# Optimization experiments

Hardware: AMD Instinct MI355X
Metric: run time of the kernel (lower is better)

The kernel has to match this reference:

```python
import jax, jax.numpy as jnp
import numpy as np

EPS = 1e-06
N_HEADS = 16


def setup_inputs() -> dict:
    key = jax.random.key(0)
    k1, k2, k3 = jax.random.split(key, 3)
    B, T, C = 2, 2048, 1024
    x = jax.random.normal(k1, (B, T, C), dtype=jnp.float32)
    Wqkv = jax.random.normal(k2, (C, 3 * C), dtype=jnp.float32) * (1.0 / np.sqrt(C))
    Wout = jax.random.normal(k3, (C, C), dtype=jnp.float32) * (1.0 / np.sqrt(C))
    return {"x": x, "Wqkv": Wqkv, "Wout": Wout}


def reference(x, Wqkv, Wout):
    B, T, C = x.shape
    H = N_HEADS
    D = C // H
    qkv = x @ Wqkv  # [B,T,3C]
    q, k, v = jnp.split(qkv, 3, axis=-1)
    # [B,H,T,D]
    q = q.reshape(B, T, H, D).transpose(0, 2, 1, 3)
    k = k.reshape(B, T, H, D).transpose(0, 2, 1, 3)
    v = v.reshape(B, T, H, D).transpose(0, 2, 1, 3)
    dot = jnp.einsum('bhqd,bhkd->bhqk', q, k)
    qn = jnp.sum(q * q, axis=-1)[..., :, None]  # [B,H,T,1]
    kn = jnp.sum(k * k, axis=-1)[..., None, :]  # [B,H,1,T]
    scores = (dot * dot) / (qn + kn - 2.0 * dot + EPS)  # score_scale == 1.0
    causal = jnp.tril(jnp.ones((T, T), dtype=bool))  # [T,T]
    scores = jnp.where(causal[None, None], scores, -jnp.inf)
    attn = jax.nn.softmax(scores, axis=-1)
    out = jnp.einsum('bhqk,bhkd->bhqd', attn, v)
    out = out.transpose(0, 2, 1, 3).reshape(B, T, C)
    return out @ Wout
```

## Files before the change

### kernel.cpp

```cpp
#include <hip/hip_runtime.h>

#define T_SEQ   2048
#define C_DIM   1024
#define B_BATCH 2
#define H_HEADS 16
#define D_HEAD  64
#define EPS_Y   1e-6f

typedef short bf16x8 __attribute__((ext_vector_type(8)));
typedef float f32x4  __attribute__((ext_vector_type(4)));

__device__ __forceinline__ void split_bf16(float f, unsigned short& h, unsigned short& l) {
  unsigned int u = __float_as_uint(f);
  unsigned int hb = (u + 0x7fffu + ((u >> 16) & 1u)) >> 16;
  h = (unsigned short)hb;
  float hf = __uint_as_float(hb << 16);
  float res = f - hf;
  unsigned int v = __float_as_uint(res);
  l = (unsigned short)((v + 0x7fffu + ((v >> 16) & 1u)) >> 16);
}
__device__ __forceinline__ float bf2f(unsigned short u) {
  return __uint_as_float((unsigned int)u << 16);
}

__global__ __launch_bounds__(256) void convert_split(
    const float* __restrict__ in, unsigned short* __restrict__ hi,
    unsigned short* __restrict__ lo, int n4) {
  int idx = blockIdx.x * 256 + threadIdx.x;
  int stride = gridDim.x * 256;
  for (int i = idx; i < n4; i += stride) {
    float4 v = ((const float4*)in)[i];
    ushort4 h, l;
    split_bf16(v.x, h.x, l.x);
    split_bf16(v.y, h.y, l.y);
    split_bf16(v.z, h.z, l.z);
    split_bf16(v.w, h.w, l.w);
    ((ushort4*)hi)[i] = h;
    ((ushort4*)lo)[i] = l;
  }
}

__global__ __launch_bounds__(256) void transpose_split(
    const float* __restrict__ W, unsigned short* __restrict__ th,
    unsigned short* __restrict__ tl, int K, int N) {
  __shared__ float tile[64][65];
  const int bk = blockIdx.y * 64;
  const int bn = blockIdx.x * 64;
  const int t  = threadIdx.x;
  const int r  = t >> 2;
  const int c0 = (t & 3) << 4;

#pragma unroll
  for (int c = 0; c < 16; c += 4) {
    float4 v = *(const float4*)(W + (size_t)(bk + r) * N + bn + c0 + c);
    tile[r][c0 + c + 0] = v.x; tile[r][c0 + c + 1] = v.y;
    tile[r][c0 + c + 2] = v.z; tile[r][c0 + c + 3] = v.w;
  }
  __syncthreads();

#pragma unroll
  for (int c = 0; c < 16; c += 4) {
    ushort4 h, l;
    split_bf16(tile[c0 + c + 0][r], h.x, l.x);
    split_bf16(tile[c0 + c + 1][r], h.y, l.y);
    split_bf16(tile[c0 + c + 2][r], h.z, l.z);
    split_bf16(tile[c0 + c + 3][r], h.w, l.w);
    size_t off = (size_t)(bn + r) * K + bk + c0 + c;
    *(ushort4*)(th + off) = h;
    *(ushort4*)(tl + off) = l;
  }
}

template <bool BF16OUT>
__global__ __launch_bounds__(256) void gemm_split(
    const unsigned short* __restrict__ Ah, const unsigned short* __restrict__ Al,
    const unsigned short* __restrict__ Bh, const unsigned short* __restrict__ Bl,
    float* __restrict__ C, unsigned short* __restrict__ Ch,
    unsigned short* __restrict__ Cl, int M, int N, int K) {
  __shared__ alignas(16) short sAh[128][32], sAl[128][32];
  __shared__ alignas(16) short sBh[128][32], sBl[128][32];
  const int t  = threadIdx.x;
  const int l  = t & 63;
  const int w  = t >> 6;
  const int bm = blockIdx.y * 128;
  const int bn = blockIdx.x * 128;
  const int wm = (w >> 1) * 64;
  const int wn = (w & 1) * 64;

  f32x4 acc[4][4] = {};

  for (int k0 = 0; k0 < K; k0 += 32) {
#pragma unroll
    for (int r = 0; r < 2; ++r) {
      const int i   = r * 256 + t;
      const int row = i >> 2;
      const int k8  = (i & 3) << 3;
      const size_t ga = (size_t)(bm + row) * K + k0 + k8;
      const size_t gb = (size_t)(bn + row) * K + k0 + k8;
      *(bf16x8*)(&sAh[row][k8]) = *(const bf16x8*)(Ah + ga);
      *(bf16x8*)(&sAl[row][k8]) = *(const bf16x8*)(Al + ga);
      *(bf16x8*)(&sBh[row][k8]) = *(const bf16x8*)(Bh + gb);
      *(bf16x8*)(&sBl[row][k8]) = *(const bf16x8*)(Bl + gb);
    }
    __syncthreads();

    bf16x8 ah[4], al4[4], bh[4], bl4[4];
    const int lr = l & 15;
    const int kk = (l >> 4) << 3;
#pragma unroll
    for (int mi = 0; mi < 4; ++mi) {
      const int row = wm + mi * 16 + lr;
      ah[mi]  = *(const bf16x8*)(&sAh[row][kk]);
      al4[mi] = *(const bf16x8*)(&sAl[row][kk]);
    }
#pragma unroll
    for (int ni = 0; ni < 4; ++ni) {
      const int row = wn + ni * 16 + lr;
      bh[ni]  = *(const bf16x8*)(&sBh[row][kk]);
      bl4[ni] = *(const bf16x8*)(&sBl[row][kk]);
    }

#pragma unroll
    for (int mi = 0; mi < 4; ++mi)
#pragma unroll
      for (int ni = 0; ni < 4; ++ni) {
        acc[mi][ni] = __builtin_amdgcn_mfma_f32_16x16x32_bf16(ah[mi],  bh[ni],  acc[mi][ni], 0, 0, 0);
        acc[mi][ni] = __builtin_amdgcn_mfma_f32_16x16x32_bf16(ah[mi],  bl4[ni], acc[mi][ni], 0, 0, 0);
        acc[mi][ni] = __builtin_amdgcn_mfma_f32_16x16x32_bf16(al4[mi], bh[ni],  acc[mi][ni], 0, 0, 0);
      }
    __syncthreads();
  }

  const int cr = (l >> 4) << 2;
  const int cc = l & 15;
#pragma unroll
  for (int mi = 0; mi < 4; ++mi)
#pragma unroll
    for (int ni = 0; ni < 4; ++ni) {
      const size_t base = (size_t)(bm + wm + mi * 16 + cr) * N + bn + wn + ni * 16 + cc;
#pragma unroll
      for (int r = 0; r < 4; ++r) {
        if constexpr (BF16OUT) {
          unsigned short hu, lu;
          split_bf16(acc[mi][ni][r], hu, lu);
          Ch[base + (size_t)r * N] = hu;
          Cl[base + (size_t)r * N] = lu;
        } else {
          C[base + (size_t)r * N] = acc[mi][ni][r];
        }
      }
    }
}

__global__ __launch_bounds__(256, 4) void yat_attn_mfma(
    const unsigned short* __restrict__ qh, const unsigned short* __restrict__ ql,
    unsigned short* __restrict__ oh, unsigned short* __restrict__ ol) {
  const int qb = blockIdx.x;
  const int bh = blockIdx.y;
  const int b  = bh >> 4;
  const int h  = bh & 15;
  const size_t rs3 = 3 * C_DIM;
  const unsigned short* baseh = qh + (size_t)b * T_SEQ * rs3;
  const unsigned short* basel = ql + (size_t)b * T_SEQ * rs3;
  const int qcol = h * D_HEAD;
  const int kcol = C_DIM + h * D_HEAD;
  const int vcol = 2 * C_DIM + h * D_HEAD;

  __shared__ alignas(16) unsigned short Kh[64][72], Kl[64][72];
  __shared__ alignas(16) unsigned short Vth[64][72], Vtl[64][72];
  __shared__ float qn_row[64], kn_row[64];

  const int t = threadIdx.x;
  const int l = t & 63;
  const int w = t >> 6;
  const int lr   = l & 15;
  const int kk0  = (l >> 4) << 3;
  const int rgrp = (l >> 4) << 2;

  {
    const int row = t >> 2;
    const int d0  = (t & 3) << 4;
    const size_t g = (size_t)(qb * 64 + row) * rs3 + qcol + d0;
    bf16x8 h0 = *(const bf16x8*)(baseh + g);
    bf16x8 h1 = *(const bf16x8*)(baseh + g + 8);
    bf16x8 l0 = *(const bf16x8*)(basel + g);
    bf16x8 l1 = *(const bf16x8*)(basel + g + 8);
    *(bf16x8*)(&Kh[row][d0])     = h0;
    *(bf16x8*)(&Kh[row][d0 + 8]) = h1;
    *(bf16x8*)(&Kl[row][d0])     = l0;
    *(bf16x8*)(&Kl[row][d0 + 8]) = l1;
    float s = 0.f;
#pragma unroll
    for (int i = 0; i < 8; ++i) {
      float f0 = bf2f((unsigned short)h0[i]) + bf2f((unsigned short)l0[i]);
      float f1 = bf2f((unsigned short)h1[i]) + bf2f((unsigned short)l1[i]);
      s = fmaf(f0, f0, s);
      s = fmaf(f1, f1, s);
    }
    s += __shfl_xor(s, 1);
    s += __shfl_xor(s, 2);
    if ((t & 3) == 0) qn_row[row] = s;
  }

  const int ar = w * 16 + lr;
  bf16x8 qa_h0 = *(const bf16x8*)(&Kh[ar][kk0]);
  bf16x8 qa_h1 = *(const bf16x8*)(&Kh[ar][32 + kk0]);
  bf16x8 qa_l0 = *(const bf16x8*)(&Kl[ar][kk0]);
  bf16x8 qa_l1 = *(const bf16x8*)(&Kl[ar][32 + kk0]);

  float m_r[4] = {-INFINITY, -INFINITY, -INFINITY, -INFINITY};
  float l_r[4] = {0.f, 0.f, 0.f, 0.f};
  f32x4 o_acc[4] = {};
  float qn4[4];
#pragma unroll
  for (int r = 0; r < 4; ++r) qn4[r] = 0.f;

  __syncthreads();
#pragma unroll
  for (int r = 0; r < 4; ++r) qn4[r] = qn_row[w * 16 + rgrp + r];

  for (int kb = 0; kb <= qb; ++kb) {
    {
      const int row = t >> 2;
      const int d0  = (t & 3) << 4;
      const size_t g = (size_t)(kb * 64 + row) * rs3 + kcol + d0;
      bf16x8 h0 = *(const bf16x8*)(baseh + g);
      bf16x8 h1 = *(const bf16x8*)(baseh + g + 8);
      bf16x8 l0 = *(const bf16x8*)(basel + g);
      bf16x8 l1 = *(const bf16x8*)(basel + g + 8);
      *(bf16x8*)(&Kh[row][d0])     = h0;
      *(bf16x8*)(&Kh[row][d0 + 8]) = h1;
      *(bf16x8*)(&Kl[row][d0])     = l0;
      *(bf16x8*)(&Kl[row][d0 + 8]) = l1;
      float s = 0.f;
#pragma unroll
      for (int i = 0; i < 8; ++i) {
        float f0 = bf2f((unsigned short)h0[i]) + bf2f((unsigned short)l0[i]);
        float f1 = bf2f((unsigned short)h1[i]) + bf2f((unsigned short)l1[i]);
        s = fmaf(f0, f0, s);
        s = fmaf(f1, f1, s);
      }
      s += __shfl_xor(s, 1);
      s += __shfl_xor(s, 2);
      if ((t & 3) == 0) kn_row[row] = s;
    }
    {
      const int vj = l;
      const int d0 = w * 16;
      const size_t g = (size_t)(kb * 64 + vj) * rs3 + vcol + d0;
      bf16x8 h0 = *(const bf16x8*)(baseh + g);
      bf16x8 h1 = *(const bf16x8*)(baseh + g + 8);
      bf16x8 l0 = *(const bf16x8*)(basel + g);
      bf16x8 l1 = *(const bf16x8*)(basel + g + 8);
#pragma unroll
      for (int i = 0; i < 8; ++i) {
        Vth[d0 + i][vj]     = (unsigned short)h0[i];
        Vth[d0 + 8 + i][vj] = (unsigned short)h1[i];
        Vtl[d0 + i][vj]     = (unsigned short)l0[i];
        Vtl[d0 + 8 + i][vj] = (unsigned short)l1[i];
      }
    }
    __syncthreads();

    f32x4 s_acc[4] = {};
#pragma unroll
    for (int jt = 0; jt < 4; ++jt) {
      const int br = jt * 16 + lr;
      bf16x8 b_h0 = *(const bf16x8*)(&Kh[br][kk0]);
      bf16x8 b_h1 = *(const bf16x8*)(&Kh[br][32 + kk0]);
      bf16x8 b_l0 = *(const bf16x8*)(&Kl[br][kk0]);
      bf16x8 b_l1 = *(const bf16x8*)(&Kl[br][32 + kk0]);
      s_acc[jt] = __builtin_amdgcn_mfma_f32_16x16x32_bf16(qa_h0, b_h0, s_acc[jt], 0, 0, 0);
      s_acc[jt] = __builtin_amdgcn_mfma_f32_16x16x32_bf16(qa_h0, b_l0, s_acc[jt], 0, 0, 0);
      s_acc[jt] = __builtin_amdgcn_mfma_f32_16x16x32_bf16(qa_l0, b_h0, s_acc[jt], 0, 0, 0);
      s_acc[jt] = __builtin_amdgcn_mfma_f32_16x16x32_bf16(qa_h1, b_h1, s_acc[jt], 0, 0, 0);
      s_acc[jt] = __builtin_amdgcn_mfma_f32_16x16x32_bf16(qa_h1, b_l1, s_acc[jt], 0, 0, 0);
      s_acc[jt] = __builtin_amdgcn_mfma_f32_16x16x32_bf16(qa_l1, b_h1, s_acc[jt], 0, 0, 0);
    }

    {
      const bool diag = (kb == qb);
      const int gq0 = qb * 64 + w * 16 + rgrp;
#pragma unroll
      for (int jt = 0; jt < 4; ++jt) {
        const float kn = kn_row[jt * 16 + lr];
        const int gk = kb * 64 + jt * 16 + lr;
#pragma unroll
        for (int r = 0; r < 4; ++r) {
          const float dot = s_acc[jt][r];
          float sc = (dot * dot) / (qn4[r] + kn - 2.f * dot + EPS_Y);
          if (diag && gk > gq0 + r) sc = -INFINITY;
          s_acc[jt][r] = sc;
        }
      }
    }

    float scale[4];
#pragma unroll
    for (int r = 0; r < 4; ++r) {
      float mm = fmaxf(fmaxf(s_acc[0][r], s_acc[1][r]),
                       fmaxf(s_acc[2][r], s_acc[3][r]));
      mm = fmaxf(mm, __shfl_xor(mm, 1));
      mm = fmaxf(mm, __shfl_xor(mm, 2));
      mm = fmaxf(mm, __shfl_xor(mm, 4));
      mm = fmaxf(mm, __shfl_xor(mm, 8));
      const float mnew = fmaxf(m_r[r], mm);
      scale[r] = __expf(m_r[r] - mnew);
      m_r[r] = mnew;
    }
#pragma unroll
    for (int r = 0; r < 4; ++r) {
      float lsum = 0.f;
#pragma unroll
      for (int jt = 0; jt < 4; ++jt) {
        float p = __expf(s_acc[jt][r] - m_r[r]);
        s_acc[jt][r] = p;
        lsum += p;
      }
      lsum += __shfl_xor(lsum, 1);
      lsum += __shfl_xor(lsum, 2);
      lsum += __shfl_xor(lsum, 4);
      lsum += __shfl_xor(lsum, 8);
      l_r[r] = l_r[r] * scale[r] + lsum;
    }
#pragma unroll
    for (int dt = 0; dt < 4; ++dt)
#pragma unroll
      for (int r = 0; r < 4; ++r) o_acc[dt][r] *= scale[r];

    __syncthreads();

#pragma unroll
    for (int jt = 0; jt < 4; ++jt)
#pragma unroll
      for (int r = 0; r < 4; ++r) {
        unsigned short hu, lu;
        split_bf16(s_acc[jt][r], hu, lu);
        const int prow = w * 16 + rgrp + r;
        Kh[prow][jt * 16 + lr] = hu;
        Kl[prow][jt * 16 + lr] = lu;
      }

    {
      bf16x8 pa_h0 = *(const bf16x8*)(&Kh[ar][kk0]);
      bf16x8 pa_h1 = *(const bf16x8*)(&Kh[ar][32 + kk0]);
      bf16x8 pa_l0 = *(const bf16x8*)(&Kl[ar][kk0]);
      bf16x8 pa_l1 = *(const bf16x8*)(&Kl[ar][32 + kk0]);
#pragma unroll
      for (int dt = 0; dt < 4; ++dt) {
        const int vr = dt * 16 + lr;
        bf16x8 v_h0 = *(const bf16x8*)(&Vth[vr][kk0]);
        bf16x8 v_h1 = *(const bf16x8*)(&Vth[vr][32 + kk0]);
        bf16x8 v_l0 = *(const bf16x8*)(&Vtl[vr][kk0]);
        bf16x8 v_l1 = *(const bf16x8*)(&Vtl[vr][32 + kk0]);
        o_acc[dt] = __builtin_amdgcn_mfma_f32_16x16x32_bf16(pa_h0, v_h0, o_acc[dt], 0, 0, 0);
        o_acc[dt] = __builtin_amdgcn_mfma_f32_16x16x32_bf16(pa_h0, v_l0, o_acc[dt], 0, 0, 0);
        o_acc[dt] = __builtin_amdgcn_mfma_f32_16x16x32_bf16(pa_l0, v_h0, o_acc[dt], 0, 0, 0);
        o_acc[dt] = __builtin_amdgcn_mfma_f32_16x16x32_bf16(pa_h1, v_h1, o_acc[dt], 0, 0, 0);
        o_acc[dt] = __builtin_amdgcn_mfma_f32_16x16x32_bf16(pa_h1, v_l1, o_acc[dt], 0, 0, 0);
        o_acc[dt] = __builtin_amdgcn_mfma_f32_16x16x32_bf16(pa_l1, v_h1, o_acc[dt], 0, 0, 0);
      }
    }
    __syncthreads();
  }

  float inv[4];
#pragma unroll
  for (int r = 0; r < 4; ++r) inv[r] = 1.f / l_r[r];
#pragma unroll
  for (int dt = 0; dt < 4; ++dt)
#pragma unroll
    for (int r = 0; r < 4; ++r) {
      float v = o_acc[dt][r] * inv[r];
      unsigned short hu, lu;
      split_bf16(v, hu, lu);
      const size_t off = ((size_t)b * T_SEQ + qb * 64 + w * 16 + rgrp + r) * C_DIM
                         + h * D_HEAD + dt * 16 + lr;
      oh[off] = hu;
      ol[off] = lu;
    }
}

extern "C" void kernel_launch(void* const* d_in, const int* in_sizes, int n_in,
                              void* d_out, int out_size, void* d_ws, size_t ws_size,
                              hipStream_t stream) {
  const float* x    = (const float*)d_in[0];
  const float* Wqkv = (const float*)d_in[1];
  const float* Wout = (const float*)d_in[2];
  float* outp = (float*)d_out;

  const int M  = B_BATCH * T_SEQ;
  const int C3 = 3 * C_DIM;

  unsigned short* xh   = (unsigned short*)d_ws;
  unsigned short* xl   = xh   + (size_t)M * C_DIM;
  unsigned short* wqh  = xl   + (size_t)M * C_DIM;
  unsigned short* wql  = wqh  + (size_t)C_DIM * C3;
  unsigned short* woh  = wql  + (size_t)C_DIM * C3;
  unsigned short* wol  = woh  + (size_t)C_DIM * C_DIM;
  unsigned short* qkvh = wol  + (size_t)C_DIM * C_DIM;
  unsigned short* qkvl = qkvh + (size_t)M * C3;
  unsigned short* ath  = qkvl + (size_t)M * C3;
  unsigned short* atl  = ath  + (size_t)M * C_DIM;

  convert_split<<<2048, 256, 0, stream>>>(x, xh, xl, M * C_DIM / 4);
  {
    dim3 g1(C3 / 64, C_DIM / 64);
    transpose_split<<<g1, 256, 0, stream>>>(Wqkv, wqh, wql, C_DIM, C3);
    dim3 g2(C_DIM / 64, C_DIM / 64);
    transpose_split<<<g2, 256, 0, stream>>>(Wout, woh, wol, C_DIM, C_DIM);
  }
  {
    dim3 grid(C3 / 128, M / 128);
    gemm_split<true><<<grid, 256, 0, stream>>>(xh, xl, wqh, wql,
                                               nullptr, qkvh, qkvl, M, C3, C_DIM);
  }
  {
    dim3 grid(T_SEQ / 64, B_BATCH * H_HEADS);
    yat_attn_mfma<<<grid, 256, 0, stream>>>(qkvh, qkvl, ath, atl);
  }
  {
    dim3 grid(C_DIM / 128, M / 128);
    gemm_split<false><<<grid, 256, 0, stream>>>(ath, atl, woh, wol,
                                                outp, nullptr, nullptr, M, C_DIM, C_DIM);
  }
  (void)in_sizes; (void)n_in; (void)out_size; (void)ws_size;
}
```

Measured before the change: 457.4 us.

## Pair causal query tiles per block and precompute row norms in separate kernel

Each attention block now processes two query tiles (qb and 31-qb) so the causal work per block is balanced, halving the grid. Query and key squared norms are computed once by a new row_norms kernel into workspace (reusing the x split buffer) instead of being recomputed per key tile in every block. Q fragments load directly from global into registers, and the score division uses a fast reciprocal. The trade-offs are fewer blocks (512) with longer serial loops, which can reduce occupancy and latency hiding, plus an extra kernel launch.

```diff
diff --git a/kernel.cpp b/kernel.cpp
--- a/kernel.cpp
+++ b/kernel.cpp
@@ -68,6 +68,39 @@
     size_t off = (size_t)(bn + r) * K + bk + c0 + c;
     *(ushort4*)(th + off) = h;
     *(ushort4*)(tl + off) = l;
+  }
+}
+
+__global__ __launch_bounds__(256) void row_norms(
+    const unsigned short* __restrict__ qkvh, const unsigned short* __restrict__ qkvl,
+    float* __restrict__ qnG, float* __restrict__ knG) {
+  const int t    = threadIdx.x;
+  const int g    = blockIdx.x * 16 + (t >> 4);
+  const int lane = t & 15;
+  const int h    = g & (H_HEADS - 1);
+  const int bt   = g >> 4;
+  const int b    = bt >> 11;
+  const int trow = bt & (T_SEQ - 1);
+  const size_t rowbase = (size_t)bt * (3 * C_DIM);
+  const size_t outi = ((size_t)(b * H_HEADS + h)) * T_SEQ + trow;
+
+#pragma unroll
+  for (int plane = 0; plane < 2; ++plane) {
+    const size_t off = rowbase + (plane ? C_DIM : 0) + h * D_HEAD + lane * 4;
+    ushort4 hh = *(const ushort4*)(qkvh + off);
+    ushort4 ll = *(const ushort4*)(qkvl + off);
+    float f0 = bf2f(hh.x) + bf2f(ll.x);
+    float f1 = bf2f(hh.y) + bf2f(ll.y);
+    float f2 = bf2f(hh.z) + bf2f(ll.z);
+    float f3 = bf2f(hh.w) + bf2f(ll.w);
+    float s = f0 * f0 + f1 * f1 + f2 * f2 + f3 * f3;
+    s += __shfl_xor(s, 1);
+    s += __shfl_xor(s, 2);
+    s += __shfl_xor(s, 4);
+    s += __shfl_xor(s, 8);
+    if (lane == 0) {
+      if (plane == 0) qnG[outi] = s; else knG[outi] = s;
+    }
   }
 }
 
@@ -154,21 +187,22 @@
 
 __global__ __launch_bounds__(256, 4) void yat_attn_mfma(
     const unsigned short* __restrict__ qh, const unsigned short* __restrict__ ql,
+    const float* __restrict__ qnG, const float* __restrict__ knG,
     unsigned short* __restrict__ oh, unsigned short* __restrict__ ol) {
-  const int qb = blockIdx.x;
-  const int bh = blockIdx.y;
-  const int b  = bh >> 4;
-  const int h  = bh & 15;
+  const int qb0 = blockIdx.x;
+  const int bh  = blockIdx.y;
+  const int b   = bh >> 4;
+  const int h   = bh & 15;
   const size_t rs3 = 3 * C_DIM;
   const unsigned short* baseh = qh + (size_t)b * T_SEQ * rs3;
   const unsigned short* basel = ql + (size_t)b * T_SEQ * rs3;
   const int qcol = h * D_HEAD;
   const int kcol = C_DIM + h * D_HEAD;
   const int vcol = 2 * C_DIM + h * D_HEAD;
+  const size_t nbase = (size_t)bh * T_SEQ;
 
   __shared__ alignas(16) unsigned short Kh[64][72], Kl[64][72];
   __shared__ alignas(16) unsigned short Vth[64][72], Vtl[64][72];
-  __shared__ float qn_row[64], kn_row[64];
 
   const int t = threadIdx.x;
   const int l = t & 63;
@@ -176,209 +210,177 @@
   const int lr   = l & 15;
   const int kk0  = (l >> 4) << 3;
   const int rgrp = (l >> 4) << 2;
-
-  {
-    const int row = t >> 2;
-    const int d0  = (t & 3) << 4;
-    const size_t g = (size_t)(qb * 64 + row) * rs3 + qcol + d0;
-    bf16x8 h0 = *(const bf16x8*)(baseh + g);
-    bf16x8 h1 = *(const bf16x8*)(baseh + g + 8);
-    bf16x8 l0 = *(const bf16x8*)(basel + g);
-    bf16x8 l1 = *(const bf16x8*)(basel + g + 8);
-    *(bf16x8*)(&Kh[row][d0])     = h0;
-    *(bf16x8*)(&Kh[row][d0 + 8]) = h1;
-    *(bf16x8*)(&Kl[row][d0])     = l0;
-    *(bf16x8*)(&Kl[row][d0 + 8]) = l1;
-    float s = 0.f;
-#pragma unroll
-    for (int i = 0; i < 8; ++i) {
-      float f0 = bf2f((unsigned short)h0[i]) + bf2f((unsigned short)l0[i]);
-      float f1 = bf2f((unsigned short)h1[i]) + bf2f((unsigned short)l1[i]);
-      s = fmaf(f0, f0, s);
-      s = fmaf(f1, f1, s);
-    }
-    s += __shfl_xor(s, 1);
-    s += __shfl_xor(s, 2);
-    if ((t & 3) == 0) qn_row[row] = s;
-  }
-
-  const int ar = w * 16 + lr;
-  bf16x8 qa_h0 = *(const bf16x8*)(&Kh[ar][kk0]);
-  bf16x8 qa_h1 = *(const bf16x8*)(&Kh[ar][32 + kk0]);
-  bf16x8 qa_l0 = *(const bf16x8*)(&Kl[ar][kk0]);
-  bf16x8 qa_l1 = *(const bf16x8*)(&Kl[ar][32 + kk0]);
-
-  float m_r[4] = {-INFINITY, -INFINITY, -INFINITY, -INFINITY};
-  float l_r[4] = {0.f, 0.f, 0.f, 0.f};
-  f32x4 o_acc[4] = {};
-  float qn4[4];
-#pragma unroll
-  for (int r = 0; r < 4; ++r) qn4[r] = 0.f;
-
-  __syncthreads();
-#pragma unroll
-  for (int r = 0; r < 4; ++r) qn4[r] = qn_row[w * 16 + rgrp + r];
-
-  for (int kb = 0; kb <= qb; ++kb) {
-    {
-      const int row = t >> 2;
-      const int d0  = (t & 3) << 4;
-      const size_t g = (size_t)(kb * 64 + row) * rs3 + kcol + d0;
-      bf16x8 h0 = *(const bf16x8*)(baseh + g);
-      bf16x8 h1 = *(const bf16x8*)(baseh + g + 8);
-      bf16x8 l0 = *(const bf16x8*)(basel + g);
-      bf16x8 l1 = *(const bf16x8*)(basel + g + 8);
-      *(bf16x8*)(&Kh[row][d0])     = h0;
-      *(bf16x8*)(&Kh[row][d0 + 8]) = h1;
-      *(bf16x8*)(&Kl[row][d0])     = l0;
-      *(bf16x8*)(&Kl[row][d0 + 8]) = l1;
-      float s = 0.f;
-#pragma unroll
-      for (int i = 0; i < 8; ++i) {
-        float f0 = bf2f((unsigned short)h0[i]) + bf2f((unsigned short)l0[i]);
-        float f1 = bf2f((unsigned short)h1[i]) + bf2f((unsigned short)l1[i]);
-        s = fmaf(f0, f0, s);
-        s = fmaf(f1, f1, s);
-      }
-      s += __shfl_xor(s, 1);
-      s += __shfl_xor(s, 2);
-      if ((t & 3) == 0) kn_row[row] = s;
-    }
-    {
-      const int vj = l;
-      const int d0 = w * 16;
-      const size_t g = (size_t)(kb * 64 + vj) * rs3 + vcol + d0;
-      bf16x8 h0 = *(const bf16x8*)(baseh + g);
-      bf16x8 h1 = *(const bf16x8*)(baseh + g + 8);
-      bf16x8 l0 = *(const bf16x8*)(basel + g);
-      bf16x8 l1 = *(const bf16x8*)(basel + g + 8);
-#pragma unroll
-      for (int i = 0; i < 8; ++i) {
-        Vth[d0 + i][vj]     = (unsigned short)h0[i];
-        Vth[d0 + 8 + i][vj] = (unsigned short)h1[i];
-        Vtl[d0 + i][vj]     = (unsigned short)l0[i];
-        Vtl[d0 + 8 + i][vj] = (unsigned short)l1[i];
-      }
-    }
-    __syncthreads();
-
-    f32x4 s_acc[4] = {};
-#pragma unroll
-    for (int jt = 0; jt < 4; ++jt) {
-      const int br = jt * 16 + lr;
-      bf16x8 b_h0 = *(const bf16x8*)(&Kh[br][kk0]);
-      bf16x8 b_h1 = *(const bf16x8*)(&Kh[br][32 + kk0]);
-      bf16x8 b_l0 = *(const bf16x8*)(&Kl[br][kk0]);
-      bf16x8 b_l1 = *(const bf16x8*)(&Kl[br][32 + kk0]);
-      s_acc[jt] = __builtin_amdgcn_mfma_f32_16x16x32_bf16(qa_h0, b_h0, s_acc[jt], 0, 0, 0);
-      s_acc[jt] = __builtin_amdgcn_mfma_f32_16x16x32_bf16(qa_h0, b_l0, s_acc[jt], 0, 0, 0);
-      s_acc[jt] = __builtin_amdgcn_mfma_f32_16x16x32_bf16(qa_l0, b_h0, s_acc[jt], 0, 0, 0);
-      s_acc[jt] = __builtin_amdgcn_mfma_f32_16x16x32_bf16(qa_h1, b_h1, s_acc[jt], 0, 0, 0);
-      s_acc[jt] = __builtin_amdgcn_mfma_f32_16x16x32_bf16(qa_h1, b_l1, s_acc[jt], 0, 0, 0);
-      s_acc[jt] = __builtin_amdgcn_mfma_f32_16x16x32_bf16(qa_l1, b_h1, s_acc[jt], 0, 0, 0);
-    }
-
-    {
-      const bool diag = (kb == qb);
-      const int gq0 = qb * 64 + w * 16 + rgrp;
+  const int ar   = w * 16 + lr;
+
+  for (int half = 0; half < 2; ++half) {
+    const int qt = half ? (31 - qb0) : qb0;
+
+    const size_t qg = (size_t)(qt * 64 + ar) * rs3 + qcol;
+    bf16x8 qa_h0 = *(const bf16x8*)(baseh + qg + kk0);
+    bf16x8 qa_h1 = *(const bf16x8*)(baseh + qg + 32 + kk0);
+    bf16x8 qa_l0 = *(const bf16x8*)(basel + qg + kk0);
+    bf16x8 qa_l1 = *(const bf16x8*)(basel + qg + 32 + kk0);
+
+    float qn4[4];
+#pragma unroll
+    for (int r = 0; r < 4; ++r)
+      qn4[r] = qnG[nbase + qt * 64 + w * 16 + rgrp + r];
+
+    float m_r[4] = {-INFINITY, -INFINITY, -INFINITY, -INFINITY};
+    float l_r[4] = {0.f, 0.f, 0.f, 0.f};
+    f32x4 o_acc[4] = {};
+
+    for (int kb = 0; kb <= qt; ++kb) {
+      {
+        const int row = t >> 2;
+        const int d0  = (t & 3) << 4;
+        const size_t g = (size_t)(kb * 64 + row) * rs3 + kcol + d0;
+        *(bf16x8*)(&Kh[row][d0])     = *(const bf16x8*)(baseh + g);
+        *(bf16x8*)(&Kh[row][d0 + 8]) = *(const bf16x8*)(baseh + g + 8);
+        *(bf16x8*)(&Kl[row][d0])     = *(const bf16x8*)(basel + g);
+        *(bf16x8*)(&Kl[row][d0 + 8]) = *(const bf16x8*)(basel + g + 8);
+      }
+      {
+        const int vj = l;
+        const int d0 = w * 16;
+        const size_t g = (size_t)(kb * 64 + vj) * rs3 + vcol + d0;
+        bf16x8 h0 = *(const bf16x8*)(baseh + g);
+        bf16x8 h1 = *(const bf16x8*)(baseh + g + 8);
+        bf16x8 l0 = *(const bf16x8*)(basel + g);
+        bf16x8 l1 = *(const bf16x8*)(basel + g + 8);
+#pragma unroll
+        for (int i = 0; i < 8; ++i) {
+          Vth[d0 + i][vj]     = (unsigned short)h0[i];
+          Vth[d0 + 8 + i][vj] = (unsigned short)h1[i];
+          Vtl[d0 + i][vj]     = (unsigned short)l0[i];
+          Vtl[d0 + 8 + i][vj] = (unsigned short)l1[i];
+        }
+      }
+      float knv[4];
+#pragma unroll
+      for (int jt = 0; jt < 4; ++jt)
+        knv[jt] = knG[nbase + kb * 64 + jt * 16 + lr];
+
+      __syncthreads();
+
+      f32x4 s_acc[4] = {};
 #pragma unroll
       for (int jt = 0; jt < 4; ++jt) {
-        const float kn = kn_row[jt * 16 + lr];
-        const int gk = kb * 64 + jt * 16 + lr;
+        const int br = jt * 16 + lr;
+        bf16x8 b_h0 = *(const bf16x8*)(&Kh[br][kk0]);
+        bf16x8 b_h1 = *(const bf16x8*)(&Kh[br][32 + kk0]);
+        bf16x8 b_l0 = *(const bf16x8*)(&Kl[br][kk0]);
+        bf16x8 b_l1 = *(const bf16x8*)(&Kl[br][32 + kk0]);
+        s_acc[jt] = __builtin_amdgcn_mfma_f32_16x16x32_bf16(qa_h0, b_h0, s_acc[jt], 0, 0, 0);
+        s_acc[jt] = __builtin_amdgcn_mfma_f32_16x16x32_bf16(qa_h0, b_l0, s_acc[jt], 0, 0, 0);
+        s_acc[jt] = __builtin_amdgcn_mfma_f32_16x16x32_bf16(qa_l0, b_h0, s_acc[jt], 0, 0, 0);
+        s_acc[jt] = __builtin_amdgcn_mfma_f32_16x16x32_bf16(qa_h1, b_h1, s_acc[jt], 0, 0, 0);
+        s_acc[jt] = __builtin_amdgcn_mfma_f32_16x16x32_bf16(qa_h1, b_l1, s_acc[jt], 0, 0, 0);
+        s_acc[jt] = __builtin_amdgcn_mfma_f32_16x16x32_bf16(qa_l1, b_h1, s_acc[jt], 0, 0, 0);
+      }
+
+      {
+        const bool diag = (kb == qt);
+        const int gq0 = qt * 64 + w * 16 + rgrp;
+#pragma unroll
+        for (int jt = 0; jt < 4; ++jt) {
+          const int gk = kb * 64 + jt * 16 + lr;
+#pragma unroll
+          for (int r = 0; r < 4; ++r) {
+            const float dot = s_acc[jt][r];
+            const float den = qn4[r] + knv[jt] - 2.f * dot + EPS_Y;
+            float sc = (dot * dot) * __builtin_amdgcn_rcpf(den);
+            if (diag && gk > gq0 + r) sc = -INFINITY;
+            s_acc[jt][r] = sc;
+          }
+        }
+      }
+
+      float scale[4];
+#pragma unroll
+      for (int r = 0; r < 4; ++r) {
+        float mm = fmaxf(fmaxf(s_acc[0][r], s_acc[1][r]),
+                         fmaxf(s_acc[2][r], s_acc[3][r]));
+        mm = fmaxf(mm, __shfl_xor(mm, 1));
+        mm = fmaxf(mm, __shfl_xor(mm, 2));
+        mm = fmaxf(mm, __shfl_xor(mm, 4));
+        mm = fmaxf(mm, __shfl_xor(mm, 8));
+        const float mnew = fmaxf(m_r[r], mm);
+        scale[r] = __expf(m_r[r] - mnew);
+        m_r[r] = mnew;
+      }
+#pragma unroll
+      for (int r = 0; r < 4; ++r) {
+        float lsum = 0.f;
+#pragma unroll
+        for (int jt = 0; jt < 4; ++jt) {
+          float p = __expf(s_acc[jt][r] - m_r[r]);
+          s_acc[jt][r] = p;
+          lsum += p;
+        }
+        lsum += __shfl_xor(lsum, 1);
+        lsum += __shfl_xor(lsum, 2);
+        lsum += __shfl_xor(lsum, 4);
+        lsum += __shfl_xor(lsum, 8);
+        l_r[r] = l_r[r] * scale[r] + lsum;
+      }
+#pragma unroll
+      for (int dt = 0; dt < 4; ++dt)
+#pragma unroll
+        for (int r = 0; r < 4; ++r) o_acc[dt][r] *= scale[r];
+
+      __syncthreads();
+
+#pragma unroll
+      for (int jt = 0; jt < 4; ++jt)
 #pragma unroll
         for (int r = 0; r < 4; ++r) {
-          const float dot = s_acc[jt][r];
-          float sc = (dot * dot) / (qn4[r] + kn - 2.f * dot + EPS_Y);
-          if (diag && gk > gq0 + r) sc = -INFINITY;
-          s_acc[jt][r] = sc;
-        }
-      }
-    }
-
-    float scale[4];
-#pragma unroll
-    for (int r = 0; r < 4; ++r) {
-      float mm = fmaxf(fmaxf(s_acc[0][r], s_acc[1][r]),
-                       fmaxf(s_acc[2][r], s_acc[3][r]));
-      mm = fmaxf(mm, __shfl_xor(mm, 1));
-      mm = fmaxf(mm, __shfl_xor(mm, 2));
-      mm = fmaxf(mm, __shfl_xor(mm, 4));
-      mm = fmaxf(mm, __shfl_xor(mm, 8));
-      const float mnew = fmaxf(m_r[r], mm);
-      scale[r] = __expf(m_r[r] - mnew);
-      m_r[r] = mnew;
-    }
-#pragma unroll
-    for (int r = 0; r < 4; ++r) {
-      float lsum = 0.f;
-#pragma unroll
-      for (int jt = 0; jt < 4; ++jt) {
-        float p = __expf(s_acc[jt][r] - m_r[r]);
-        s_acc[jt][r] = p;
-        lsum += p;
-      }
-      lsum += __shfl_xor(lsum, 1);
-      lsum += __shfl_xor(lsum, 2);
-      lsum += __shfl_xor(lsum, 4);
-      lsum += __shfl_xor(lsum, 8);
-      l_r[r] = l_r[r] * scale[r] + lsum;
-    }
+          unsigned short hu, lu;
+          split_bf16(s_acc[jt][r], hu, lu);
+          const int prow = w * 16 + rgrp + r;
+          Kh[prow][jt * 16 + lr] = hu;
+          Kl[prow][jt * 16 + lr] = lu;
+        }
+
+      {
+        bf16x8 pa_h0 = *(const bf16x8*)(&Kh[ar][kk0]);
+        bf16x8 pa_h1 = *(const bf16x8*)(&Kh[ar][32 + kk0]);
+        bf16x8 pa_l0 = *(const bf16x8*)(&Kl[ar][kk0]);
+        bf16x8 pa_l1 = *(const bf16x8*)(&Kl[ar][32 + kk0]);
+#pragma unroll
+        for (int dt = 0; dt < 4; ++dt) {
+          const int vr = dt * 16 + lr;
+          bf16x8 v_h0 = *(const bf16x8*)(&Vth[vr][kk0]);
+          bf16x8 v_h1 = *(const bf16x8*)(&Vth[vr][32 + kk0]);
+          bf16x8 v_l0 = *(const bf16x8*)(&Vtl[vr][kk0]);
+          bf16x8 v_l1 = *(const bf16x8*)(&Vtl[vr][32 + kk0]);
+          o_acc[dt] = __builtin_amdgcn_mfma_f32_16x16x32_bf16(pa_h0, v_h0, o_acc[dt], 0, 0, 0);
+          o_acc[dt] = __builtin_amdgcn_mfma_f32_16x16x32_bf16(pa_h0, v_l0, o_acc[dt], 0, 0, 0);
+          o_acc[dt] = __builtin_amdgcn_mfma_f32_16x16x32_bf16(pa_l0, v_h0, o_acc[dt], 0, 0, 0);
+          o_acc[dt] = __builtin_amdgcn_mfma_f32_16x16x32_bf16(pa_h1, v_h1, o_acc[dt], 0, 0, 0);
+          o_acc[dt] = __builtin_amdgcn_mfma_f32_16x16x32_bf16(pa_h1, v_l1, o_acc[dt], 0, 0, 0);
+          o_acc[dt] = __builtin_amdgcn_mfma_f32_16x16x32_bf16(pa_l1, v_h1, o_acc[dt], 0, 0, 0);
+        }
+      }
+      __syncthreads();
+    }
+
+    float inv[4];
+#pragma unroll
+    for (int r = 0; r < 4; ++r) inv[r] = 1.f / l_r[r];
 #pragma unroll
     for (int dt = 0; dt < 4; ++dt)
 #pragma unroll
-      for (int r = 0; r < 4; ++r) o_acc[dt][r] *= scale[r];
-
-    __syncthreads();
-
-#pragma unroll
-    for (int jt = 0; jt < 4; ++jt)
-#pragma unroll
       for (int r = 0; r < 4; ++r) {
+        float v = o_acc[dt][r] * inv[r];
         unsigned short hu, lu;
-        split_bf16(s_acc[jt][r], hu, lu);
-        const int prow = w * 16 + rgrp + r;
-        Kh[prow][jt * 16 + lr] = hu;
-        Kl[prow][jt * 16 + lr] = lu;
-      }
-
-    {
-      bf16x8 pa_h0 = *(const bf16x8*)(&Kh[ar][kk0]);
-      bf16x8 pa_h1 = *(const bf16x8*)(&Kh[ar][32 + kk0]);
-      bf16x8 pa_l0 = *(const bf16x8*)(&Kl[ar][kk0]);
-      bf16x8 pa_l1 = *(const bf16x8*)(&Kl[ar][32 + kk0]);
-#pragma unroll
-      for (int dt = 0; dt < 4; ++dt) {
-        const int vr = dt * 16 + lr;
-        bf16x8 v_h0 = *(const bf16x8*)(&Vth[vr][kk0]);
-        bf16x8 v_h1 = *(const bf16x8*)(&Vth[vr][32 + kk0]);
-        bf16x8 v_l0 = *(const bf16x8*)(&Vtl[vr][kk0]);
-        bf16x8 v_l1 = *(const bf16x8*)(&Vtl[vr][32 + kk0]);
-        o_acc[dt] = __builtin_amdgcn_mfma_f32_16x16x32_bf16(pa_h0, v_h0, o_acc[dt], 0, 0, 0);
-        o_acc[dt] = __builtin_amdgcn_mfma_f32_16x16x32_bf16(pa_h0, v_l0, o_acc[dt], 0, 0, 0);
-        o_acc[dt] = __builtin_amdgcn_mfma_f32_16x16x32_bf16(pa_l0, v_h0, o_acc[dt], 0, 0, 0);
-        o_acc[dt] = __builtin_amdgcn_mfma_f32_16x16x32_bf16(pa_h1, v_h1, o_acc[dt], 0, 0, 0);
-        o_acc[dt] = __builtin_amdgcn_mfma_f32_16x16x32_bf16(pa_h1, v_l1, o_acc[dt], 0, 0, 0);
-        o_acc[dt] = __builtin_amdgcn_mfma_f32_16x16x32_bf16(pa_l1, v_h1, o_acc[dt], 0, 0, 0);
-      }
-    }
-    __syncthreads();
-  }
-
-  float inv[4];
-#pragma unroll
-  for (int r = 0; r < 4; ++r) inv[r] = 1.f / l_r[r];
-#pragma unroll
-  for (int dt = 0; dt < 4; ++dt)
-#pragma unroll
-    for (int r = 0; r < 4; ++r) {
-      float v = o_acc[dt][r] * inv[r];
-      unsigned short hu, lu;
-      split_bf16(v, hu, lu);
-      const size_t off = ((size_t)b * T_SEQ + qb * 64 + w * 16 + rgrp + r) * C_DIM
-                         + h * D_HEAD + dt * 16 + lr;
-      oh[off] = hu;
-      ol[off] = lu;
-    }
+        split_bf16(v, hu, lu);
+        const size_t off = ((size_t)b * T_SEQ + qt * 64 + w * 16 + rgrp + r) * C_DIM
+                           + h * D_HEAD + dt * 16 + lr;
+        oh[off] = hu;
+        ol[off] = lu;
+      }
+  }
 }
 
 extern "C" void kernel_launch(void* const* d_in, const int* in_sizes, int n_in,
@@ -402,6 +404,8 @@
   unsigned short* qkvl = qkvh + (size_t)M * C3;
   unsigned short* ath  = qkvl + (size_t)M * C3;
   unsigned short* atl  = ath  + (size_t)M * C_DIM;
+  float* qnG = (float*)xh;
+  float* knG = qnG + (size_t)B_BATCH * H_HEADS * T_SEQ;
 
   convert_split<<<2048, 256, 0, stream>>>(x, xh, xl, M * C_DIM / 4);
   {
@@ -415,9 +419,10 @@
     gemm_split<true><<<grid, 256, 0, stream>>>(xh, xl, wqh, wql,
                                                nullptr, qkvh, qkvl, M, C3, C_DIM);
   }
+  row_norms<<<M * H_HEADS / 16, 256, 0, stream>>>(qkvh, qkvl, qnG, knG);
   {
-    dim3 grid(T_SEQ / 64, B_BATCH * H_HEADS);
-    yat_attn_mfma<<<grid, 256, 0, stream>>>(qkvh, qkvl, ath, atl);
+    dim3 grid(T_SEQ / 64 / 2, B_BATCH * H_HEADS);
+    yat_attn_mfma<<<grid, 256, 0, stream>>>(qkvh, qkvl, qnG, knG, ath, atl);
   }
   {
     dim3 grid(C_DIM / 128, M / 128);
```

After: 393.1 us. -14.1%, faster.
